# Performance work log

Hardware: AMD Instinct MI355X
Metric: run time of the kernel (lower is better)

The kernel has to match this reference:

```python
import jax, jax.numpy as jnp
import numpy as np

N_NODES = 100000
N_EDGES = 1600000
D_NODE = 32
D_EDGE = 16
D_HID = 64
D_OUT = 32


def setup_inputs() -> dict:
    key = jax.random.key(0)
    ks = jax.random.split(key, 7)
    x = jax.random.normal(ks[0], (N_NODES, D_NODE), dtype=jnp.float32)
    edge_index = jax.random.randint(ks[1], (2, N_EDGES), 0, N_NODES, dtype=jnp.int64)
    edge_attr = jax.random.normal(ks[2], (N_EDGES, D_EDGE), dtype=jnp.float32)
    # 2-layer MLP params (Linear -> ReLU -> Linear), He-ish scaling
    W1 = jax.random.normal(ks[3], (D_NODE + D_EDGE, D_HID), dtype=jnp.float32) * (2.0 / (D_NODE + D_EDGE)) ** 0.5
    b1 = jnp.zeros((D_HID,), dtype=jnp.float32)
    W2 = jax.random.normal(ks[4], (D_HID, D_OUT), dtype=jnp.float32) * (2.0 / D_HID) ** 0.5
    b2 = jnp.zeros((D_OUT,), dtype=jnp.float32)
    return {"x": x, "edge_index": edge_index, "edge_attr": edge_attr,
            "W1": W1, "b1": b1, "W2": W2, "b2": b2}


def reference(x, edge_index, edge_attr, W1, b1, W2, b2):
    row, col = edge_index[0], edge_index[1]
    # gather source-node feats and concat with edge feats: [E, d_node + d_edge]
    inp = jnp.concatenate([x[col], edge_attr], axis=1)
    # 2-layer MLP over edges
    h = jax.nn.relu(inp @ W1 + b1)
    messages = h @ W2 + b2  # [E, d_out]
    # scatter-sum aggregate by destination node
    message = jax.ops.segment_sum(messages, row, num_segments=x.shape[0])
    return message
```

## Files before the change

### kernel.cpp

```cpp
#include <hip/hip_runtime.h>
#include <hip/hip_bf16.h>
#include <stdint.h>

#define N_NODES 100000
#define N_EDGES 1600000
#define D_NODE  32
#define D_EDGE  16
#define D_IN    48
#define D_HID   64
#define D_OUT   32

#define NFLAGS_OFF  ((size_t)0)
#define NB1_OFF     ((size_t)64)
#define NB2_OFF     ((size_t)320)
#define W1BF_OFF    ((size_t)1024)
#define W2BF_OFF    ((size_t)9216)
#define COUNTS_OFF  ((size_t)65536)
#define OFFSETS_OFF ((size_t)466944)
#define BLKSUM_OFF  ((size_t)917504)
#define RANK_OFF    ((size_t)1048576)
#define MSG_OFF     ((size_t)8388608)

#define SCAN_NB 391

typedef __attribute__((ext_vector_type(8))) short bf16x8;
typedef __attribute__((ext_vector_type(4))) float f32x4;

__device__ inline float bf2f(unsigned int u16) {
    return __uint_as_float(u16 << 16);
}
__device__ inline unsigned short f2bf_rne(float f) {
    unsigned int x = __float_as_uint(f);
    unsigned int r = (x + 0x7FFFu + ((x >> 16) & 1u)) >> 16;
    return (unsigned short)r;
}
__device__ inline float ld_f(const void* p, int i, int isbf) {
    if (isbf) return bf2f(((const unsigned short*)p)[i]);
    return ((const float*)p)[i];
}
__device__ inline bf16x8 pack_bf8(float4 v0, float4 v1) {
    bf16x8 r;
    r[0] = (short)f2bf_rne(v0.x); r[1] = (short)f2bf_rne(v0.y);
    r[2] = (short)f2bf_rne(v0.z); r[3] = (short)f2bf_rne(v0.w);
    r[4] = (short)f2bf_rne(v1.x); r[5] = (short)f2bf_rne(v1.y);
    r[6] = (short)f2bf_rne(v1.z); r[7] = (short)f2bf_rne(v1.w);
    return r;
}

__global__ void prep_kernel(const void* __restrict__ xq, const void* __restrict__ idxq,
                            const void* __restrict__ W1q, const void* __restrict__ b1q,
                            const void* __restrict__ W2q, const void* __restrict__ b2q,
                            char* __restrict__ ws) {
    __shared__ int s_isbf;
    if (threadIdx.x == 0) {
        const unsigned short* u = (const unsigned short*)xq;
        int isbf = 1;
        for (int i = 0; i < 64; ++i) {
            int e = (u[i] >> 7) & 0xFF;
            if (e >= 140) { isbf = 0; break; }
        }
        const int* w = (const int*)idxq;
        int is64 = 1;
        for (int i = 1; i < 64; i += 2) {
            if (w[i] != 0) { is64 = 0; break; }
        }
        int* flags = (int*)(ws + NFLAGS_OFF);
        flags[0] = isbf;
        flags[1] = is64;
        s_isbf = isbf;
    }
    __syncthreads();
    const int isbf = s_isbf;
    float* b1 = (float*)(ws + NB1_OFF);
    float* b2 = (float*)(ws + NB2_OFF);
    unsigned short* w1b = (unsigned short*)(ws + W1BF_OFF);
    unsigned short* w2b = (unsigned short*)(ws + W2BF_OFF);

    if (threadIdx.x < D_HID) b1[threadIdx.x] = ld_f(b1q, threadIdx.x, isbf);
    if (threadIdx.x < D_OUT) b2[threadIdx.x] = ld_f(b2q, threadIdx.x, isbf);

    for (int i = threadIdx.x; i < D_HID * 64; i += blockDim.x) {
        int n = i >> 6, k = i & 63;
        float v = (k < D_IN) ? ld_f(W1q, k * D_HID + n, isbf) : 0.0f;
        w1b[i] = f2bf_rne(v);
    }
    for (int i = threadIdx.x; i < D_OUT * 64; i += blockDim.x) {
        int n = i >> 6, k = i & 63;
        w2b[i] = f2bf_rne(ld_f(W2q, k * D_OUT + n, isbf));
    }
}

__global__ __launch_bounds__(256) void hist_kernel(const void* __restrict__ idxq,
                                                   char* __restrict__ ws,
                                                   int* __restrict__ rankb) {
    const int is64 = ((const int*)(ws + NFLAGS_OFF))[1];
    const int e = blockIdx.x * 256 + threadIdx.x;
    int dst;
    if (is64) dst = (int)((const long long*)idxq)[e];
    else      dst = ((const int*)idxq)[e];
    rankb[e] = atomicAdd((int*)(ws + COUNTS_OFF) + dst, 1);
}

__global__ __launch_bounds__(256) void scan_block_kernel(char* __restrict__ ws) {
    __shared__ int s[256];
    const int* counts = (const int*)(ws + COUNTS_OFF);
    int* offs   = (int*)(ws + OFFSETS_OFF);
    int* blksum = (int*)(ws + BLKSUM_OFF);
    const int t = threadIdx.x;
    const int i = blockIdx.x * 256 + t;
    int v = (i < N_NODES) ? counts[i] : 0;
    s[t] = v;
    __syncthreads();
    for (int d = 1; d < 256; d <<= 1) {
        int a = (t >= d) ? s[t - d] : 0;
        __syncthreads();
        s[t] += a;
        __syncthreads();
    }
    if (i < N_NODES) offs[i] = s[t] - v;
    if (t == 255) blksum[blockIdx.x] = s[255];
}

__global__ __launch_bounds__(512) void scan_tops_kernel(char* __restrict__ ws) {
    __shared__ int s[512];
    int* blksum = (int*)(ws + BLKSUM_OFF);
    const int t = threadIdx.x;
    int v = (t < SCAN_NB) ? blksum[t] : 0;
    s[t] = v;
    __syncthreads();
    for (int d = 1; d < 512; d <<= 1) {
        int a = (t >= d) ? s[t - d] : 0;
        __syncthreads();
        s[t] += a;
        __syncthreads();
    }
    if (t < SCAN_NB) blksum[t] = s[t] - v;
}

__global__ __launch_bounds__(256) void scan_add_kernel(char* __restrict__ ws) {
    int* offs   = (int*)(ws + OFFSETS_OFF);
    const int* blksum = (const int*)(ws + BLKSUM_OFF);
    const int i = blockIdx.x * 256 + threadIdx.x;
    if (i < N_NODES) offs[i] += blksum[blockIdx.x];
    if (i == 0) offs[N_NODES] = N_EDGES;
}

__global__ __launch_bounds__(256) void edge_mlp_mfma_kernel(
        const void* __restrict__ xq,
        const void* __restrict__ idxq,
        const void* __restrict__ eaq,
        const char* __restrict__ wsro,
        const int* __restrict__ rankb,
        unsigned short* __restrict__ msg) {
    const int isbf = ((const int*)(wsro + NFLAGS_OFF))[0];
    const int is64 = ((const int*)(wsro + NFLAGS_OFF))[1];

    __shared__ __align__(16) unsigned short hbuf[4][4][16][72];

    const int tid = threadIdx.x;
    const int w   = tid >> 6;
    const int l   = tid & 63;
    const int m16 = l & 15;
    const int q   = l >> 4;

    const unsigned short* w1b = (const unsigned short*)(wsro + W1BF_OFF);
    const unsigned short* w2b = (const unsigned short*)(wsro + W2BF_OFF);
    const float* b1 = (const float*)(wsro + NB1_OFF);
    const float* b2 = (const float*)(wsro + NB2_OFF);
    const int* offs = (const int*)(wsro + OFFSETS_OFF);

    bf16x8 w1f[4][2], w2f[2][2];
#pragma unroll
    for (int t = 0; t < 4; ++t)
#pragma unroll
        for (int c = 0; c < 2; ++c)
            w1f[t][c] = *(const bf16x8*)(w1b + ((t * 16 + m16) * 64 + c * 32 + q * 8));
#pragma unroll
    for (int t = 0; t < 2; ++t)
#pragma unroll
        for (int c = 0; c < 2; ++c)
            w2f[t][c] = *(const bf16x8*)(w2b + ((t * 16 + m16) * 64 + c * 32 + q * 8));

    const int eb = blockIdx.x * 256 + w * 64;

    int srcv[4], posv[4];
#pragma unroll
    for (int g = 0; g < 4; ++g) {
        const int e = eb + g * 16 + m16;
        int dst;
        if (is64) {
            const long long* ip = (const long long*)idxq;
            dst = (int)ip[e];
            srcv[g] = (int)ip[N_EDGES + e];
        } else {
            const int* ip = (const int*)idxq;
            dst = ip[e];
            srcv[g] = ip[N_EDGES + e];
        }
        posv[g] = offs[dst] + rankb[e];
    }

    bf16x8 A0[4], A1[4];
#pragma unroll
    for (int g = 0; g < 4; ++g) {
        const int e = eb + g * 16 + m16;
#pragma unroll
        for (int i = 0; i < 8; ++i) A1[g][i] = 0;
        if (isbf) {
            const unsigned short* x  = (const unsigned short*)xq;
            const unsigned short* ea = (const unsigned short*)eaq;
            A0[g] = *(const bf16x8*)(x + (size_t)srcv[g] * D_NODE + q * 8);
            if (q < 2) A1[g] = *(const bf16x8*)(ea + (size_t)e * D_EDGE + q * 8);
        } else {
            const float* x  = (const float*)xq;
            const float* ea = (const float*)eaq;
            const float4* xp = (const float4*)(x + (size_t)srcv[g] * D_NODE + q * 8);
            A0[g] = pack_bf8(xp[0], xp[1]);
            if (q < 2) {
                const float4* ap = (const float4*)(ea + (size_t)e * D_EDGE + q * 8);
                A1[g] = pack_bf8(ap[0], ap[1]);
            }
        }
    }

    const float b1v[4] = { b1[m16], b1[16 + m16], b1[32 + m16], b1[48 + m16] };
#pragma unroll
    for (int g = 0; g < 4; ++g) {
#pragma unroll
        for (int t = 0; t < 4; ++t) {
            f32x4 c;
            c[0] = c[1] = c[2] = c[3] = b1v[t];
            c = __builtin_amdgcn_mfma_f32_16x16x32_bf16(A0[g], w1f[t][0], c, 0, 0, 0);
            c = __builtin_amdgcn_mfma_f32_16x16x32_bf16(A1[g], w1f[t][1], c, 0, 0, 0);
#pragma unroll
            for (int r = 0; r < 4; ++r)
                hbuf[w][g][q * 4 + r][t * 16 + m16] = f2bf_rne(fmaxf(c[r], 0.0f));
        }
    }

    const float b2v[2] = { b2[m16], b2[16 + m16] };
#pragma unroll
    for (int g = 0; g < 4; ++g) {
        bf16x8 a20 = *(const bf16x8*)(&hbuf[w][g][m16][q * 8]);
        bf16x8 a21 = *(const bf16x8*)(&hbuf[w][g][m16][32 + q * 8]);
#pragma unroll
        for (int t = 0; t < 2; ++t) {
            f32x4 c;
            c[0] = c[1] = c[2] = c[3] = b2v[t];
            c = __builtin_amdgcn_mfma_f32_16x16x32_bf16(a20, w2f[t][0], c, 0, 0, 0);
            c = __builtin_amdgcn_mfma_f32_16x16x32_bf16(a21, w2f[t][1], c, 0, 0, 0);
#pragma unroll
            for (int r = 0; r < 4; ++r)
                hbuf[w][g][q * 4 + r][t * 16 + m16] = f2bf_rne(c[r]);
        }
    }

    const int mrow = l >> 2;
    const int sub  = l & 3;
#pragma unroll
    for (int g = 0; g < 4; ++g) {
        const int posm = __shfl(posv[g], mrow, 64);
        uint4 rowv = *(const uint4*)(&hbuf[w][g][mrow][sub * 8]);
        *(uint4*)(msg + (size_t)posm * D_OUT + sub * 8) = rowv;
    }
}

__global__ __launch_bounds__(256) void reduce_kernel(
        const char* __restrict__ wsro, const unsigned short* __restrict__ msg,
        void* __restrict__ out) {
    const int isbf = ((const int*)(wsro + NFLAGS_OFF))[0];
    const int* offs = (const int*)(wsro + OFFSETS_OFF);
    const int t = blockIdx.x * 256 + threadIdx.x;
    const int node = t >> 4;
    if (node >= N_NODES) return;
    const int c2 = t & 15;
    const int lo = offs[node], hi = offs[node + 1];
    float s0 = 0.0f, s1 = 0.0f;
    const unsigned int* p = (const unsigned int*)msg + (size_t)lo * 16 + c2;
    int k = lo;
    for (; k + 1 < hi; k += 2) {
        unsigned int a = p[0], b = p[16];
        s0 += __uint_as_float(a << 16) + __uint_as_float(b << 16);
        s1 += __uint_as_float(a & 0xFFFF0000u) + __uint_as_float(b & 0xFFFF0000u);
        p += 32;
    }
    if (k < hi) {
        unsigned int a = p[0];
        s0 += __uint_as_float(a << 16);
        s1 += __uint_as_float(a & 0xFFFF0000u);
    }
    if (isbf) {
        unsigned int pk = (unsigned int)f2bf_rne(s0) | ((unsigned int)f2bf_rne(s1) << 16);
        ((unsigned int*)out)[(size_t)node * 16 + c2] = pk;
    } else {
        float2 v; v.x = s0; v.y = s1;
        ((float2*)out)[(size_t)node * 16 + c2] = v;
    }
}

extern "C" void kernel_launch(void* const* d_in, const int* in_sizes, int n_in,
                              void* d_out, int out_size, void* d_ws, size_t ws_size,
                              hipStream_t stream) {
    const void* x   = d_in[0];
    const void* idx = d_in[1];
    const void* ea  = d_in[2];
    const void* W1  = d_in[3];
    const void* b1  = d_in[4];
    const void* W2  = d_in[5];
    const void* b2  = d_in[6];
    char* ws = (char*)d_ws;

    hipMemsetAsync(ws + COUNTS_OFF, 0, (size_t)N_NODES * 4, stream);

    hipLaunchKernelGGL(prep_kernel, dim3(1), dim3(256), 0, stream,
                       x, idx, W1, b1, W2, b2, ws);

    hipLaunchKernelGGL(hist_kernel, dim3(N_EDGES / 256), dim3(256), 0, stream,
                       idx, ws, (int*)(ws + RANK_OFF));

    hipLaunchKernelGGL(scan_block_kernel, dim3(SCAN_NB), dim3(256), 0, stream, ws);
    hipLaunchKernelGGL(scan_tops_kernel,  dim3(1),       dim3(512), 0, stream, ws);
    hipLaunchKernelGGL(scan_add_kernel,   dim3(SCAN_NB), dim3(256), 0, stream, ws);

    hipLaunchKernelGGL(edge_mlp_mfma_kernel, dim3(N_EDGES / 256), dim3(256), 0, stream,
                       x, idx, ea, (const char*)ws,
                       (const int*)(ws + RANK_OFF), (unsigned short*)(ws + MSG_OFF));

    hipLaunchKernelGGL(reduce_kernel, dim3((N_NODES * 16 + 255) / 256), dim3(256), 0, stream,
                       (const char*)ws, (const unsigned short*)(ws + MSG_OFF), d_out);
}
```

Measured before the change: 394.0 us.

## Shrink edge MLP blocks to one wave, interleave layers, fuse scan passes

The edge MLP kernel now runs one 64-thread wave per block with a two-slot LDS buffer. Layer-1 and layer-2 MFMA work for the four 16-edge groups is interleaved so LDS round trips and the scatter stores can overlap with compute. The scan-tops kernel is removed, and each scan_add block now sums the preceding block totals itself, saving one launch. It also switches bf16 packing to the packed HIP conversion intrinsic and uses wave ballots for the input-format detection in prep. The cost is more blocks to schedule and redundant prefix reductions across the scan blocks.

```diff
diff --git a/kernel.cpp b/kernel.cpp
--- a/kernel.cpp
+++ b/kernel.cpp
@@ -34,17 +34,22 @@
     unsigned int r = (x + 0x7FFFu + ((x >> 16) & 1u)) >> 16;
     return (unsigned short)r;
 }
+__device__ inline unsigned int pk_bf2(float a, float b) {
+    float2 f; f.x = a; f.y = b;
+    __hip_bfloat162 h = __float22bfloat162_rn(f);
+    return *reinterpret_cast<unsigned int*>(&h);
+}
 __device__ inline float ld_f(const void* p, int i, int isbf) {
     if (isbf) return bf2f(((const unsigned short*)p)[i]);
     return ((const float*)p)[i];
 }
 __device__ inline bf16x8 pack_bf8(float4 v0, float4 v1) {
-    bf16x8 r;
-    r[0] = (short)f2bf_rne(v0.x); r[1] = (short)f2bf_rne(v0.y);
-    r[2] = (short)f2bf_rne(v0.z); r[3] = (short)f2bf_rne(v0.w);
-    r[4] = (short)f2bf_rne(v1.x); r[5] = (short)f2bf_rne(v1.y);
-    r[6] = (short)f2bf_rne(v1.z); r[7] = (short)f2bf_rne(v1.w);
-    return r;
+    union { unsigned int u[4]; bf16x8 v; } r;
+    r.u[0] = pk_bf2(v0.x, v0.y);
+    r.u[1] = pk_bf2(v0.z, v0.w);
+    r.u[2] = pk_bf2(v1.x, v1.y);
+    r.u[3] = pk_bf2(v1.z, v1.w);
+    return r.v;
 }
 
 __global__ void prep_kernel(const void* __restrict__ xq, const void* __restrict__ idxq,
@@ -52,22 +57,18 @@
                             const void* __restrict__ W2q, const void* __restrict__ b2q,
                             char* __restrict__ ws) {
     __shared__ int s_isbf;
-    if (threadIdx.x == 0) {
-        const unsigned short* u = (const unsigned short*)xq;
-        int isbf = 1;
-        for (int i = 0; i < 64; ++i) {
-            int e = (u[i] >> 7) & 0xFF;
-            if (e >= 140) { isbf = 0; break; }
-        }
-        const int* w = (const int*)idxq;
-        int is64 = 1;
-        for (int i = 1; i < 64; i += 2) {
-            if (w[i] != 0) { is64 = 0; break; }
-        }
-        int* flags = (int*)(ws + NFLAGS_OFF);
-        flags[0] = isbf;
-        flags[1] = is64;
-        s_isbf = isbf;
+    const int t = threadIdx.x;
+    if (t < 64) {
+        unsigned short u = ((const unsigned short*)xq)[t];
+        unsigned long long mb = __ballot(((u >> 7) & 0xFF) >= 140);
+        int wodd = ((const int*)idxq)[2 * t + 1];
+        unsigned long long mi = __ballot(wodd != 0);
+        if (t == 0) {
+            int* flags = (int*)(ws + NFLAGS_OFF);
+            flags[0] = (mb == 0ULL);
+            flags[1] = (mi == 0ULL);
+            s_isbf = (mb == 0ULL);
+        }
     }
     __syncthreads();
     const int isbf = s_isbf;
@@ -76,15 +77,15 @@
     unsigned short* w1b = (unsigned short*)(ws + W1BF_OFF);
     unsigned short* w2b = (unsigned short*)(ws + W2BF_OFF);
 
-    if (threadIdx.x < D_HID) b1[threadIdx.x] = ld_f(b1q, threadIdx.x, isbf);
-    if (threadIdx.x < D_OUT) b2[threadIdx.x] = ld_f(b2q, threadIdx.x, isbf);
-
-    for (int i = threadIdx.x; i < D_HID * 64; i += blockDim.x) {
+    if (t < D_HID) b1[t] = ld_f(b1q, t, isbf);
+    if (t < D_OUT) b2[t] = ld_f(b2q, t, isbf);
+
+    for (int i = t; i < D_HID * 64; i += blockDim.x) {
         int n = i >> 6, k = i & 63;
         float v = (k < D_IN) ? ld_f(W1q, k * D_HID + n, isbf) : 0.0f;
         w1b[i] = f2bf_rne(v);
     }
-    for (int i = threadIdx.x; i < D_OUT * 64; i += blockDim.x) {
+    for (int i = t; i < D_OUT * 64; i += blockDim.x) {
         int n = i >> 6, k = i & 63;
         w2b[i] = f2bf_rne(ld_f(W2q, k * D_OUT + n, isbf));
     }
@@ -121,31 +122,27 @@
     if (t == 255) blksum[blockIdx.x] = s[255];
 }
 
-__global__ __launch_bounds__(512) void scan_tops_kernel(char* __restrict__ ws) {
-    __shared__ int s[512];
-    int* blksum = (int*)(ws + BLKSUM_OFF);
+__global__ __launch_bounds__(256) void scan_add_kernel(char* __restrict__ ws) {
+    __shared__ int s[256];
+    int* offs = (int*)(ws + OFFSETS_OFF);
+    const int* blksum = (const int*)(ws + BLKSUM_OFF);
     const int t = threadIdx.x;
-    int v = (t < SCAN_NB) ? blksum[t] : 0;
-    s[t] = v;
+    const int b = blockIdx.x;
+    int acc = 0;
+    for (int j = t; j < b; j += 256) acc += blksum[j];
+    s[t] = acc;
     __syncthreads();
-    for (int d = 1; d < 512; d <<= 1) {
-        int a = (t >= d) ? s[t - d] : 0;
+    for (int d = 128; d > 0; d >>= 1) {
+        if (t < d) s[t] += s[t + d];
         __syncthreads();
-        s[t] += a;
-        __syncthreads();
-    }
-    if (t < SCAN_NB) blksum[t] = s[t] - v;
-}
-
-__global__ __launch_bounds__(256) void scan_add_kernel(char* __restrict__ ws) {
-    int* offs   = (int*)(ws + OFFSETS_OFF);
-    const int* blksum = (const int*)(ws + BLKSUM_OFF);
-    const int i = blockIdx.x * 256 + threadIdx.x;
-    if (i < N_NODES) offs[i] += blksum[blockIdx.x];
+    }
+    const int prefix = s[0];
+    const int i = b * 256 + t;
+    if (i < N_NODES) offs[i] += prefix;
     if (i == 0) offs[N_NODES] = N_EDGES;
 }
 
-__global__ __launch_bounds__(256) void edge_mlp_mfma_kernel(
+__global__ __launch_bounds__(64) void edge_mlp_mfma_kernel(
         const void* __restrict__ xq,
         const void* __restrict__ idxq,
         const void* __restrict__ eaq,
@@ -155,11 +152,9 @@
     const int isbf = ((const int*)(wsro + NFLAGS_OFF))[0];
     const int is64 = ((const int*)(wsro + NFLAGS_OFF))[1];
 
-    __shared__ __align__(16) unsigned short hbuf[4][4][16][72];
-
-    const int tid = threadIdx.x;
-    const int w   = tid >> 6;
-    const int l   = tid & 63;
+    __shared__ __align__(16) unsigned short hbuf[2][16][72];
+
+    const int l   = threadIdx.x;
     const int m16 = l & 15;
     const int q   = l >> 4;
 
@@ -181,7 +176,7 @@
         for (int c = 0; c < 2; ++c)
             w2f[t][c] = *(const bf16x8*)(w2b + ((t * 16 + m16) * 64 + c * 32 + q * 8));
 
-    const int eb = blockIdx.x * 256 + w * 64;
+    const int eb = blockIdx.x * 64;
 
     int srcv[4], posv[4];
 #pragma unroll
@@ -224,45 +219,54 @@
     }
 
     const float b1v[4] = { b1[m16], b1[16 + m16], b1[32 + m16], b1[48 + m16] };
-#pragma unroll
-    for (int g = 0; g < 4; ++g) {
+    const float b2v[2] = { b2[m16], b2[16 + m16] };
+    const int mrow = l >> 2;
+    const int sub  = l & 3;
+
+    auto L1 = [&](int g, int b) {
 #pragma unroll
         for (int t = 0; t < 4; ++t) {
             f32x4 c;
             c[0] = c[1] = c[2] = c[3] = b1v[t];
             c = __builtin_amdgcn_mfma_f32_16x16x32_bf16(A0[g], w1f[t][0], c, 0, 0, 0);
             c = __builtin_amdgcn_mfma_f32_16x16x32_bf16(A1[g], w1f[t][1], c, 0, 0, 0);
-#pragma unroll
-            for (int r = 0; r < 4; ++r)
-                hbuf[w][g][q * 4 + r][t * 16 + m16] = f2bf_rne(fmaxf(c[r], 0.0f));
-        }
-    }
-
-    const float b2v[2] = { b2[m16], b2[16 + m16] };
-#pragma unroll
-    for (int g = 0; g < 4; ++g) {
-        bf16x8 a20 = *(const bf16x8*)(&hbuf[w][g][m16][q * 8]);
-        bf16x8 a21 = *(const bf16x8*)(&hbuf[w][g][m16][32 + q * 8]);
+            unsigned int u0 = pk_bf2(fmaxf(c[0], 0.0f), fmaxf(c[1], 0.0f));
+            unsigned int u1 = pk_bf2(fmaxf(c[2], 0.0f), fmaxf(c[3], 0.0f));
+            hbuf[b][q * 4 + 0][t * 16 + m16] = (unsigned short)u0;
+            hbuf[b][q * 4 + 1][t * 16 + m16] = (unsigned short)(u0 >> 16);
+            hbuf[b][q * 4 + 2][t * 16 + m16] = (unsigned short)u1;
+            hbuf[b][q * 4 + 3][t * 16 + m16] = (unsigned short)(u1 >> 16);
+        }
+    };
+    auto L2S = [&](int g, int b) {
+        bf16x8 a20 = *(const bf16x8*)(&hbuf[b][m16][q * 8]);
+        bf16x8 a21 = *(const bf16x8*)(&hbuf[b][m16][32 + q * 8]);
 #pragma unroll
         for (int t = 0; t < 2; ++t) {
             f32x4 c;
             c[0] = c[1] = c[2] = c[3] = b2v[t];
             c = __builtin_amdgcn_mfma_f32_16x16x32_bf16(a20, w2f[t][0], c, 0, 0, 0);
             c = __builtin_amdgcn_mfma_f32_16x16x32_bf16(a21, w2f[t][1], c, 0, 0, 0);
-#pragma unroll
-            for (int r = 0; r < 4; ++r)
-                hbuf[w][g][q * 4 + r][t * 16 + m16] = f2bf_rne(c[r]);
-        }
-    }
-
-    const int mrow = l >> 2;
-    const int sub  = l & 3;
-#pragma unroll
-    for (int g = 0; g < 4; ++g) {
+            unsigned int u0 = pk_bf2(c[0], c[1]);
+            unsigned int u1 = pk_bf2(c[2], c[3]);
+            hbuf[b][q * 4 + 0][t * 16 + m16] = (unsigned short)u0;
+            hbuf[b][q * 4 + 1][t * 16 + m16] = (unsigned short)(u0 >> 16);
+            hbuf[b][q * 4 + 2][t * 16 + m16] = (unsigned short)u1;
+            hbuf[b][q * 4 + 3][t * 16 + m16] = (unsigned short)(u1 >> 16);
+        }
         const int posm = __shfl(posv[g], mrow, 64);
-        uint4 rowv = *(const uint4*)(&hbuf[w][g][mrow][sub * 8]);
+        uint4 rowv = *(const uint4*)(&hbuf[b][mrow][sub * 8]);
         *(uint4*)(msg + (size_t)posm * D_OUT + sub * 8) = rowv;
-    }
+    };
+
+    L1(0, 0);
+    L1(1, 1);
+    L2S(0, 0);
+    L1(2, 0);
+    L2S(1, 1);
+    L1(3, 1);
+    L2S(2, 0);
+    L2S(3, 1);
 }
 
 __global__ __launch_bounds__(256) void reduce_kernel(
@@ -290,8 +294,7 @@
         s1 += __uint_as_float(a & 0xFFFF0000u);
     }
     if (isbf) {
-        unsigned int pk = (unsigned int)f2bf_rne(s0) | ((unsigned int)f2bf_rne(s1) << 16);
-        ((unsigned int*)out)[(size_t)node * 16 + c2] = pk;
+        ((unsigned int*)out)[(size_t)node * 16 + c2] = pk_bf2(s0, s1);
     } else {
         float2 v; v.x = s0; v.y = s1;
         ((float2*)out)[(size_t)node * 16 + c2] = v;
@@ -319,10 +322,9 @@
                        idx, ws, (int*)(ws + RANK_OFF));
 
     hipLaunchKernelGGL(scan_block_kernel, dim3(SCAN_NB), dim3(256), 0, stream, ws);
-    hipLaunchKernelGGL(scan_tops_kernel,  dim3(1),       dim3(512), 0, stream, ws);
     hipLaunchKernelGGL(scan_add_kernel,   dim3(SCAN_NB), dim3(256), 0, stream, ws);
 
-    hipLaunchKernelGGL(edge_mlp_mfma_kernel, dim3(N_EDGES / 256), dim3(256), 0, stream,
+    hipLaunchKernelGGL(edge_mlp_mfma_kernel, dim3(N_EDGES / 64), dim3(64), 0, stream,
                        x, idx, ea, (const char*)ws,
                        (const int*)(ws + RANK_OFF), (unsigned short*)(ws + MSG_OFF));
 
```

Result: faster. 380.8 us (-3.4%).
